# Optimization experiments

Hardware: AMD Instinct MI355X
Metric: run time of the kernel (lower is better)

## Reference

```python
import jax, jax.numpy as jnp
import numpy as np

N = 100000   # nodes
E = 1000000  # edges (avg degree 10)
F_IN, H1, H2, C = 128, 64, 64, 16


def setup_inputs() -> dict:
    key = jax.random.key(0)
    ks = jax.random.split(key, 10)
    x = jax.random.normal(ks[0], (N, F_IN), dtype=jnp.float32)
    edge_src = jax.random.randint(ks[1], (E,), 0, N, dtype=jnp.int32)
    edge_dst = jax.random.randint(ks[2], (E,), 0, N, dtype=jnp.int32)
    # normalized-adjacency-like positive edge weights (~1/deg scale)
    edge_val = jax.random.uniform(ks[3], (E,), dtype=jnp.float32) * 0.1
    def glorot(k, fan_in, fan_out):
        s = np.float32(1.0 / np.sqrt(fan_in))
        return jax.random.normal(k, (fan_in, fan_out), dtype=jnp.float32) * s
    W1 = glorot(ks[4], F_IN, H1)
    W2 = glorot(ks[5], H1, H2)
    W3 = glorot(ks[6], H2, C)
    b1 = jnp.zeros((H1,), jnp.float32)
    b2 = jnp.zeros((H2,), jnp.float32)
    b3 = jnp.zeros((C,), jnp.float32)
    return {"x": x, "edge_val": edge_val, "W1": W1, "b1": b1,
            "W2": W2, "b2": b2, "W3": W3, "b3": b3,
            "edge_src": edge_src, "edge_dst": edge_dst}


def gcn_layer(h, W, b, edge_src, edge_dst, edge_val):
    # support = h @ W ; out = spmm(adj, support) + b
    support = h @ W                                  # [N, d_out]
    msg = support[edge_src] * edge_val[:, None]      # [E, d_out] gather + scale
    agg = jax.ops.segment_sum(msg, edge_dst, num_segments=N)  # scatter-add
    return agg + b


def reference(x, edge_val, W1, b1, W2, b2, W3, b3, edge_src, edge_dst):
    # eval mode: F.dropout(training=False) is identity
    h = jax.nn.relu(gcn_layer(x, W1, b1, edge_src, edge_dst, edge_val))
    h = jax.nn.relu(gcn_layer(h, W2, b2, edge_src, edge_dst, edge_val))
    return gcn_layer(h, W3, b3, edge_src, edge_dst, edge_val)  # [N, C] logits
```

## Files before the change

kernel.cpp:

```cpp
#include <hip/hip_runtime.h>
#include <stdint.h>

#define N_NODES 100000
#define N_EDGES 1000000
#define NBUCK 98

typedef __attribute__((ext_vector_type(8))) __bf16 bf16x8;
typedef __attribute__((ext_vector_type(4))) float f32x4;

static __device__ __forceinline__ float bf2f(unsigned short u) {
    return __uint_as_float(((unsigned int)u) << 16);
}
static __device__ __forceinline__ unsigned short f2bf(float f) {
    unsigned int u = __float_as_uint(f);
    unsigned int r = (u + 0x7FFFu + ((u >> 16) & 1u)) >> 16;
    return (unsigned short)r;
}
static __device__ __forceinline__ float4 ld4_half(const unsigned short* p) {
    ushort4 u = *(const ushort4*)p;
    return make_float4(bf2f(u.x), bf2f(u.y), bf2f(u.z), bf2f(u.w));
}
static __device__ __forceinline__ void st4_half(unsigned short* p, float4 f) {
    ushort4 u;
    u.x = f2bf(f.x); u.y = f2bf(f.y); u.z = f2bf(f.z); u.w = f2bf(f.w);
    *(ushort4*)p = u;
}

static __device__ __forceinline__ float ldf(const void* p, size_t i, int bf) {
    return bf ? bf2f(((const unsigned short*)p)[i]) : ((const float*)p)[i];
}
static __device__ __forceinline__ float4 ldf4(const void* p, size_t i, int bf) {
    if (bf) return ld4_half((const unsigned short*)p + i);
    return *(const float4*)((const float*)p + i);
}

__global__ __launch_bounds__(256) void detect_kernel(const unsigned short* __restrict__ xs,
                                                     int* __restrict__ flag) {
    __shared__ int sz;
    if (threadIdx.x == 0) sz = 0;
    __syncthreads();
    int z = 0;
    for (int i = threadIdx.x; i < 1024; i += 256) {
        float av = fabsf(bf2f(xs[2 * i]));
        if (!(av <= 1048576.0f) || (av != 0.0f && av < 9.5367431640625e-07f)) z++;
    }
    atomicAdd(&sz, z);
    __syncthreads();
    if (threadIdx.x == 0) *flag = (sz > 256) ? 0 : 1;
}

__global__ __launch_bounds__(256) void bhist_kernel(const int* __restrict__ dst,
                                                    int* __restrict__ bcount) {
    __shared__ int cnt[NBUCK];
    int tid = threadIdx.x;
    for (int i = tid; i < NBUCK; i += 256) cnt[i] = 0;
    __syncthreads();
    int e0 = blockIdx.x * 4096;
#pragma unroll
    for (int i = 0; i < 16; ++i) {
        int e = e0 + i * 256 + tid;
        if (e < N_EDGES) atomicAdd(&cnt[dst[e] >> 10], 1);
    }
    __syncthreads();
    for (int i = tid; i < NBUCK; i += 256) {
        int c = cnt[i];
        if (c) atomicAdd(&bcount[i], c);
    }
}

__global__ __launch_bounds__(128) void bscan_kernel(const int* __restrict__ bcount,
                                                    int* __restrict__ bstart,
                                                    int* __restrict__ bcursor) {
    __shared__ int sh[128];
    int tid = threadIdx.x;
    int v = (tid < NBUCK) ? bcount[tid] : 0;
    sh[tid] = v;
    __syncthreads();
    for (int off = 1; off < 128; off <<= 1) {
        int t = 0;
        if (tid >= off) t = sh[tid - off];
        __syncthreads();
        if (tid >= off) sh[tid] += t;
        __syncthreads();
    }
    if (tid < NBUCK) {
        int excl = sh[tid] - v;
        bstart[tid] = excl;
        bcursor[tid] = excl;
    }
    if (tid == NBUCK - 1) bstart[NBUCK] = sh[tid];
}

__global__ __launch_bounds__(256) void part_kernel(const int* __restrict__ src,
                                                   const int* __restrict__ dst,
                                                   const void* __restrict__ val,
                                                   int* __restrict__ bcursor,
                                                   int2* __restrict__ part,
                                                   const int* __restrict__ flagp) {
    __shared__ int cnt[NBUCK];
    __shared__ int base[NBUCK];
    const int bf = *flagp;
    const int tid = threadIdx.x;
    const int e0 = blockIdx.x * 2048;
    for (int i = tid; i < NBUCK; i += 256) cnt[i] = 0;
    __syncthreads();
    int rank[8], bkt[8], pk[8], vb[8];
#pragma unroll
    for (int i = 0; i < 8; ++i) {
        int e = e0 + i * 256 + tid;
        bkt[i] = -1;
        if (e < N_EDGES) {
            int d = dst[e];
            int b = d >> 10;
            bkt[i] = b;
            pk[i] = src[e] | ((d & 1023) << 17);
            vb[i] = __float_as_int(ldf(val, e, bf));
            rank[i] = atomicAdd(&cnt[b], 1);
        }
    }
    __syncthreads();
    for (int i = tid; i < NBUCK; i += 256) {
        int c = cnt[i];
        base[i] = c ? atomicAdd(&bcursor[i], c) : 0;
    }
    __syncthreads();
#pragma unroll
    for (int i = 0; i < 8; ++i) {
        if (bkt[i] >= 0) part[(size_t)base[bkt[i]] + rank[i]] = make_int2(pk[i], vb[i]);
    }
}

__global__ __launch_bounds__(512) void place_kernel(const int* __restrict__ bstart,
                                                    const int2* __restrict__ part,
                                                    int* __restrict__ row_start,
                                                    int2* __restrict__ csr_rec) {
    __shared__ int cnt[1024];
    __shared__ int sums[512];
    const int tid = threadIdx.x;
    const int b = blockIdx.x;
    const int row0 = b << 10;
    const int nrows = min(1024, N_NODES - row0);
    const int s = bstart[b], e = bstart[b + 1];

    for (int i = tid; i < 1024; i += 512) cnt[i] = 0;
    __syncthreads();
    for (int j = s + tid; j < e; j += 512) {
        unsigned p = (unsigned)part[j].x;
        atomicAdd(&cnt[p >> 17], 1);
    }
    __syncthreads();
    int a0 = cnt[2 * tid], a1 = cnt[2 * tid + 1];
    int ts = a0 + a1;
    sums[tid] = ts;
    __syncthreads();
    for (int off = 1; off < 512; off <<= 1) {
        int t = 0;
        if (tid >= off) t = sums[tid - off];
        __syncthreads();
        if (tid >= off) sums[tid] += t;
        __syncthreads();
    }
    int excl = sums[tid] - ts;
    cnt[2 * tid] = s + excl;
    cnt[2 * tid + 1] = s + excl + a0;
    if (2 * tid < nrows)     row_start[row0 + 2 * tid] = s + excl;
    if (2 * tid + 1 < nrows) row_start[row0 + 2 * tid + 1] = s + excl + a0;
    if (b == NBUCK - 1 && tid == 0) row_start[N_NODES] = e;
    __syncthreads();
    for (int j = s + tid; j < e; j += 512) {
        int2 r = part[j];
        unsigned p = (unsigned)r.x;
        int pos = atomicAdd(&cnt[p >> 17], 1);
        csr_rec[pos] = make_int2((int)(p & 0x1FFFFu), r.y);
    }
}

template <int K, int M, bool DYNIN>
__global__ __launch_bounds__(256) void mgemm_kernel(const void* __restrict__ hv_,
                                                    const void* __restrict__ W,
                                                    unsigned short* __restrict__ out,
                                                    const int* __restrict__ flagp) {
    constexpr int LROWS = 64;
    constexpr int KP = K + 8;
    constexpr int NC = M / 16;

    __shared__ unsigned short hs[LROWS][KP];
    __shared__ unsigned short wt[M][KP];

    const int bf = *flagp;
    const int tid = threadIdx.x;
    const int base = blockIdx.x * LROWS;

    for (int i = tid; i < K * M; i += 256) {
        int k = i / M, m = i % M;
        wt[m][k] = f2bf(ldf(W, i, bf));
    }
    for (int i = tid * 4; i < LROWS * K; i += 1024) {
        int r = i / K;
        int kk = i & (K - 1);
        int grow = base + r;
        ushort4 u = make_ushort4(0, 0, 0, 0);
        if (grow < N_NODES) {
            if (DYNIN) {
                float4 f = ldf4(hv_, (size_t)grow * K + kk, bf);
                u.x = f2bf(f.x); u.y = f2bf(f.y); u.z = f2bf(f.z); u.w = f2bf(f.w);
            } else {
                u = *(const ushort4*)((const unsigned short*)hv_ + (size_t)grow * K + kk);
            }
        }
        *(ushort4*)&hs[r][kk] = u;
    }
    __syncthreads();

    const int wave = tid >> 6;
    const int lane = tid & 63;
    const int qd = lane >> 4;
    const int ln = lane & 15;
    const int wrow = wave * 16;

    f32x4 acc[NC];
#pragma unroll
    for (int c = 0; c < NC; ++c) acc[c] = (f32x4){0.f, 0.f, 0.f, 0.f};

#pragma unroll
    for (int k0 = 0; k0 < K; k0 += 32) {
        bf16x8 a = *(const bf16x8*)&hs[wrow + ln][k0 + qd * 8];
#pragma unroll
        for (int c = 0; c < NC; ++c) {
            bf16x8 b = *(const bf16x8*)&wt[c * 16 + ln][k0 + qd * 8];
            acc[c] = __builtin_amdgcn_mfma_f32_16x16x32_bf16(a, b, acc[c], 0, 0, 0);
        }
    }

#pragma unroll
    for (int c = 0; c < NC; ++c) {
#pragma unroll
        for (int r = 0; r < 4; ++r) {
            int row = base + wrow + qd * 4 + r;
            if (row < N_NODES) out[(size_t)row * M + c * 16 + ln] = f2bf(acc[c][r]);
        }
    }
}

template <int M, bool RELU, bool DYNOUT>
__global__ __launch_bounds__(256) void spmm_kernel(const unsigned short* __restrict__ support,
                                                   const int* __restrict__ row_start,
                                                   const int2* __restrict__ csr_rec,
                                                   const void* __restrict__ bias,
                                                   void* __restrict__ out_,
                                                   const int* __restrict__ flagp) {
    constexpr int GROUP = M / 4;
    constexpr int GPB = 256 / GROUP;
    int bf = *flagp;
    int tid = threadIdx.x;
    int gid = blockIdx.x * GPB + tid / GROUP;
    int c0 = (tid % GROUP) * 4;
    if (gid >= N_NODES) return;
    int s = row_start[gid];
    int e = row_start[gid + 1];
    float a0 = ldf(bias, c0 + 0, bf);
    float a1 = ldf(bias, c0 + 1, bf);
    float a2 = ldf(bias, c0 + 2, bf);
    float a3 = ldf(bias, c0 + 3, bf);
    const unsigned short* supc = support + c0;

    int j = s;
    for (; j + 3 < e; j += 4) {
        int2 r0 = csr_rec[j + 0];
        int2 r1 = csr_rec[j + 1];
        int2 r2 = csr_rec[j + 2];
        int2 r3 = csr_rec[j + 3];
        float4 s0 = ld4_half(supc + (size_t)r0.x * M);
        float4 s1 = ld4_half(supc + (size_t)r1.x * M);
        float4 s2 = ld4_half(supc + (size_t)r2.x * M);
        float4 s3 = ld4_half(supc + (size_t)r3.x * M);
        float v0 = __int_as_float(r0.y);
        float v1 = __int_as_float(r1.y);
        float v2 = __int_as_float(r2.y);
        float v3 = __int_as_float(r3.y);
        a0 += v0 * s0.x; a1 += v0 * s0.y; a2 += v0 * s0.z; a3 += v0 * s0.w;
        a0 += v1 * s1.x; a1 += v1 * s1.y; a2 += v1 * s1.z; a3 += v1 * s1.w;
        a0 += v2 * s2.x; a1 += v2 * s2.y; a2 += v2 * s2.z; a3 += v2 * s2.w;
        a0 += v3 * s3.x; a1 += v3 * s3.y; a2 += v3 * s3.z; a3 += v3 * s3.w;
    }
    for (; j < e; ++j) {
        int2 rec = csr_rec[j];
        float v = __int_as_float(rec.y);
        float4 sp = ld4_half(supc + (size_t)rec.x * M);
        a0 += v * sp.x; a1 += v * sp.y; a2 += v * sp.z; a3 += v * sp.w;
    }
    if (RELU) {
        a0 = fmaxf(a0, 0.f); a1 = fmaxf(a1, 0.f);
        a2 = fmaxf(a2, 0.f); a3 = fmaxf(a3, 0.f);
    }
    float4 f = make_float4(a0, a1, a2, a3);
    if (DYNOUT) {
        if (bf) st4_half((unsigned short*)out_ + (size_t)gid * M + c0, f);
        else    *(float4*)((float*)out_ + (size_t)gid * M + c0) = f;
    } else {
        st4_half((unsigned short*)out_ + (size_t)gid * M + c0, f);
    }
}

extern "C" void kernel_launch(void* const* d_in, const int* in_sizes, int n_in,
                              void* d_out, int out_size, void* d_ws, size_t ws_size,
                              hipStream_t stream) {
    (void)in_sizes; (void)n_in; (void)out_size; (void)ws_size;
    const void* x  = d_in[0];
    const void* ev = d_in[1];
    const void* W1 = d_in[2];
    const void* b1 = d_in[3];
    const void* W2 = d_in[4];
    const void* b2 = d_in[5];
    const void* W3 = d_in[6];
    const void* b3 = d_in[7];
    const int* esrc = (const int*)d_in[8];
    const int* edst = (const int*)d_in[9];

    char* ws = (char*)d_ws;
    size_t off = 0;
    auto alloc = [&](size_t bytes) -> void* {
        void* p = ws + off;
        off = (off + bytes + 255) & ~(size_t)255;
        return p;
    };
    unsigned short* A = (unsigned short*)alloc((size_t)N_NODES * 64 * 2);
    unsigned short* B = (unsigned short*)alloc((size_t)N_NODES * 64 * 2);
    int* row_start  = (int*)alloc((size_t)(N_NODES + 1) * 4);
    int* bcount     = (int*)alloc(512);
    int* bstart     = (int*)alloc(512);
    int* bcursor    = (int*)alloc(512);
    int2* csr_rec   = (int2*)alloc((size_t)N_EDGES * 8);
    int* flagp      = (int*)alloc(256);
    int2* part      = (int2*)A;

    detect_kernel<<<1, 256, 0, stream>>>((const unsigned short*)x, flagp);

    hipMemsetAsync(bcount, 0, 512, stream);
    bhist_kernel<<<(N_EDGES + 4095) / 4096, 256, 0, stream>>>(edst, bcount);
    bscan_kernel<<<1, 128, 0, stream>>>(bcount, bstart, bcursor);
    part_kernel<<<(N_EDGES + 2047) / 2048, 256, 0, stream>>>(esrc, edst, ev, bcursor, part, flagp);
    place_kernel<<<NBUCK, 512, 0, stream>>>(bstart, part, row_start, csr_rec);

    int gm  = (N_NODES + 63) / 64;
    int gs64 = (N_NODES + 15) / 16;

    mgemm_kernel<128, 64, true><<<gm, 256, 0, stream>>>(x, W1, A, flagp);
    spmm_kernel<64, true, false><<<gs64, 256, 0, stream>>>(A, row_start, csr_rec, b1, B, flagp);
    mgemm_kernel<64, 64, false><<<gm, 256, 0, stream>>>(B, W2, A, flagp);
    spmm_kernel<64, true, false><<<gs64, 256, 0, stream>>>(A, row_start, csr_rec, b2, B, flagp);
    mgemm_kernel<64, 16, false><<<gm, 256, 0, stream>>>(B, W3, A, flagp);
    spmm_kernel<16, false, true><<<gm, 256, 0, stream>>>(A, row_start, csr_rec, b3, d_out, flagp);
}
```

Before: 282.1 us.

## Make mgemm persistent with register-resident weight fragments and direct global A loads

```diff
diff --git a/kernel.cpp b/kernel.cpp
--- a/kernel.cpp
+++ b/kernel.cpp
@@ -176,68 +176,78 @@
 }
 
 template <int K, int M, bool DYNIN>
-__global__ __launch_bounds__(256) void mgemm_kernel(const void* __restrict__ hv_,
-                                                    const void* __restrict__ W,
-                                                    unsigned short* __restrict__ out,
-                                                    const int* __restrict__ flagp) {
-    constexpr int LROWS = 64;
+__global__ __launch_bounds__(256, 4) void mgemm_kernel(const void* __restrict__ hv_,
+                                                       const void* __restrict__ W,
+                                                       unsigned short* __restrict__ out,
+                                                       const int* __restrict__ flagp) {
     constexpr int KP = K + 8;
     constexpr int NC = M / 16;
-
-    __shared__ unsigned short hs[LROWS][KP];
+    constexpr int NK = K / 32;
+    constexpr int NT = (N_NODES + 63) / 64;
+
     __shared__ unsigned short wt[M][KP];
 
     const int bf = *flagp;
     const int tid = threadIdx.x;
-    const int base = blockIdx.x * LROWS;
 
     for (int i = tid; i < K * M; i += 256) {
         int k = i / M, m = i % M;
         wt[m][k] = f2bf(ldf(W, i, bf));
     }
-    for (int i = tid * 4; i < LROWS * K; i += 1024) {
-        int r = i / K;
-        int kk = i & (K - 1);
-        int grow = base + r;
-        ushort4 u = make_ushort4(0, 0, 0, 0);
-        if (grow < N_NODES) {
-            if (DYNIN) {
-                float4 f = ldf4(hv_, (size_t)grow * K + kk, bf);
-                u.x = f2bf(f.x); u.y = f2bf(f.y); u.z = f2bf(f.z); u.w = f2bf(f.w);
-            } else {
-                u = *(const ushort4*)((const unsigned short*)hv_ + (size_t)grow * K + kk);
-            }
-        }
-        *(ushort4*)&hs[r][kk] = u;
-    }
-    __syncthreads();
-
-    const int wave = tid >> 6;
+    __syncthreads();
+
     const int lane = tid & 63;
     const int qd = lane >> 4;
     const int ln = lane & 15;
-    const int wrow = wave * 16;
-
-    f32x4 acc[NC];
-#pragma unroll
-    for (int c = 0; c < NC; ++c) acc[c] = (f32x4){0.f, 0.f, 0.f, 0.f};
-
-#pragma unroll
-    for (int k0 = 0; k0 < K; k0 += 32) {
-        bf16x8 a = *(const bf16x8*)&hs[wrow + ln][k0 + qd * 8];
+    const int wrow = (tid >> 6) * 16;
+
+    bf16x8 bfrag[NK][NC];
+#pragma unroll
+    for (int ks = 0; ks < NK; ++ks)
+#pragma unroll
+        for (int c = 0; c < NC; ++c)
+            bfrag[ks][c] = *(const bf16x8*)&wt[c * 16 + ln][ks * 32 + qd * 8];
+
+    for (int tile = blockIdx.x; tile < NT; tile += gridDim.x) {
+        const int row = tile * 64 + wrow + ln;
+        const bool ok = row < N_NODES;
+
+        f32x4 acc[NC];
+#pragma unroll
+        for (int c = 0; c < NC; ++c) acc[c] = (f32x4){0.f, 0.f, 0.f, 0.f};
+
+#pragma unroll
+        for (int ks = 0; ks < NK; ++ks) {
+            bf16x8 a;
+            if (ok) {
+                const size_t base = (size_t)row * K + ks * 32 + qd * 8;
+                if (DYNIN && !bf) {
+                    const float* xp = (const float*)hv_ + base;
+                    float4 f0 = *(const float4*)xp;
+                    float4 f1 = *(const float4*)(xp + 4);
+                    ushort4 u0, u1;
+                    u0.x = f2bf(f0.x); u0.y = f2bf(f0.y); u0.z = f2bf(f0.z); u0.w = f2bf(f0.w);
+                    u1.x = f2bf(f1.x); u1.y = f2bf(f1.y); u1.z = f2bf(f1.z); u1.w = f2bf(f1.w);
+                    ushort4 uu[2] = {u0, u1};
+                    a = *(const bf16x8*)uu;
+                } else {
+                    a = *(const bf16x8*)((const unsigned short*)hv_ + base);
+                }
+            } else {
+                a = (bf16x8)(__bf16)0.0f;
+            }
+#pragma unroll
+            for (int c = 0; c < NC; ++c)
+                acc[c] = __builtin_amdgcn_mfma_f32_16x16x32_bf16(a, bfrag[ks][c], acc[c], 0, 0, 0);
+        }
+
 #pragma unroll
         for (int c = 0; c < NC; ++c) {
-            bf16x8 b = *(const bf16x8*)&wt[c * 16 + ln][k0 + qd * 8];
-            acc[c] = __builtin_amdgcn_mfma_f32_16x16x32_bf16(a, b, acc[c], 0, 0, 0);
-        }
-    }
-
-#pragma unroll
-    for (int c = 0; c < NC; ++c) {
-#pragma unroll
-        for (int r = 0; r < 4; ++r) {
-            int row = base + wrow + qd * 4 + r;
-            if (row < N_NODES) out[(size_t)row * M + c * 16 + ln] = f2bf(acc[c][r]);
+#pragma unroll
+            for (int r = 0; r < 4; ++r) {
+                int orow = tile * 64 + wrow + qd * 4 + r;
+                if (orow < N_NODES) out[(size_t)orow * M + c * 16 + ln] = f2bf(acc[c][r]);
+            }
         }
     }
 }
@@ -342,13 +352,14 @@
     part_kernel<<<(N_EDGES + 2047) / 2048, 256, 0, stream>>>(esrc, edst, ev, bcursor, part, flagp);
     place_kernel<<<NBUCK, 512, 0, stream>>>(bstart, part, row_start, csr_rec);
 
-    int gm  = (N_NODES + 63) / 64;
+    int gm   = 1024;
     int gs64 = (N_NODES + 15) / 16;
+    int g64  = (N_NODES + 63) / 64;
 
     mgemm_kernel<128, 64, true><<<gm, 256, 0, stream>>>(x, W1, A, flagp);
     spmm_kernel<64, true, false><<<gs64, 256, 0, stream>>>(A, row_start, csr_rec, b1, B, flagp);
     mgemm_kernel<64, 64, false><<<gm, 256, 0, stream>>>(B, W2, A, flagp);
     spmm_kernel<64, true, false><<<gs64, 256, 0, stream>>>(A, row_start, csr_rec, b2, B, flagp);
     mgemm_kernel<64, 16, false><<<gm, 256, 0, stream>>>(B, W3, A, flagp);
-    spmm_kernel<16, false, true><<<gm, 256, 0, stream>>>(A, row_start, csr_rec, b3, d_out, flagp);
-}
+    spmm_kernel<16, false, true><<<g64, 256, 0, stream>>>(A, row_start, csr_rec, b3, d_out, flagp);
+}
```

New measurement: 277.3 us. No clear change (-1.7%).
